# Performance work log

Hardware: AMD Instinct MI355X
Metric: run time of the kernel (lower is better)

The kernel has to match this reference:

```python
import jax, jax.numpy as jnp
import numpy as np

B, T, D = 2, 2048, 1024
NH, DH = 16, 64  # inner = NH*DH = D
SCALE_INIT = 0.02


def setup_inputs() -> dict:
    key = jax.random.key(0)
    kx, kq, kk, kv, ko = jax.random.split(key, 5)
    return {
        "x": jax.random.normal(kx, (B, T, D), dtype=jnp.float32),
        "Wq": jax.random.normal(kq, (D, NH * DH), dtype=jnp.float32) * SCALE_INIT,
        "Wk": jax.random.normal(kk, (D, NH * DH), dtype=jnp.float32) * SCALE_INIT,
        "Wv": jax.random.normal(kv, (D, NH * DH), dtype=jnp.float32) * SCALE_INIT,
        "Wo": jax.random.normal(ko, (NH * DH, D), dtype=jnp.float32) * SCALE_INIT,
    }


def reference(x, Wq, Wk, Wv, Wo):
    # x: (B, T, D)
    b, t, _ = x.shape

    def split_heads(h):
        # (B, T, NH*DH) -> (B, NH, T, DH)
        return h.reshape(b, t, NH, DH).transpose(0, 2, 1, 3)

    q = split_heads(x @ Wq)
    k = split_heads(x @ Wk)
    v = split_heads(x @ Wv)

    scale = jnp.asarray(1.0 / np.sqrt(DH), dtype=x.dtype)
    # The per-chunk loop in the original is mathematically equivalent to
    # full causal attention: each query row attends to keys with k_pos <= q_pos.
    scores = jnp.einsum("bhqd,bhkd->bhqk", q, k) * scale  # (B, NH, T, T)
    causal_mask = jnp.arange(t)[None, :] > jnp.arange(t)[:, None]  # k_pos > q_pos
    scores = jnp.where(causal_mask, -jnp.inf, scores)
    attn = jax.nn.softmax(scores, axis=-1)
    attn = jnp.nan_to_num(attn)  # matches torch.nan_to_num (no fully-masked rows in causal case)
    o = jnp.einsum("bhqk,bhkd->bhqd", attn, v)  # (B, NH, T, DH)
    o = o.transpose(0, 2, 1, 3).reshape(b, t, NH * DH)  # merge heads
    return o @ Wo  # (B, T, D)
```

## Files before the change

### kernel.cpp

```cpp
#include <hip/hip_runtime.h>
#include <hip/hip_bf16.h>
#include <string.h>

#define Bsz 2
#define Tsz 2048
#define Dsz 1024
#define NHsz 16
#define Msz (Bsz*Tsz)

typedef unsigned short bfu;
typedef __attribute__((ext_vector_type(8))) short short8;
typedef __attribute__((ext_vector_type(4))) short short4v;
typedef __attribute__((ext_vector_type(4))) float floatx4;

__device__ __forceinline__ bfu f2bf(float f) {
  unsigned int u = __builtin_bit_cast(unsigned int, f);
  u += 0x7fffu + ((u >> 16) & 1u);
  return (bfu)(u >> 16);
}

__device__ __forceinline__ float fexp2(float x) {
#if __has_builtin(__builtin_amdgcn_exp2f)
  return __builtin_amdgcn_exp2f(x);
#else
  return exp2f(x);
#endif
}

__device__ __forceinline__ short4v pack4bf(float a, float b, float c_, float d) {
  __hip_bfloat162 h01 = __float22bfloat162_rn(make_float2(a, b));
  __hip_bfloat162 h23 = __float22bfloat162_rn(make_float2(c_, d));
  uint2 uu;
  memcpy(&uu.x, &h01, 4);
  memcpy(&uu.y, &h23, 4);
  return __builtin_bit_cast(short4v, uu);
}

__device__ __forceinline__ short8 pack8bf(float4 a, float4 b) {
  __hip_bfloat162 h0 = __float22bfloat162_rn(make_float2(a.x, a.y));
  __hip_bfloat162 h1 = __float22bfloat162_rn(make_float2(a.z, a.w));
  __hip_bfloat162 h2 = __float22bfloat162_rn(make_float2(b.x, b.y));
  __hip_bfloat162 h3 = __float22bfloat162_rn(make_float2(b.z, b.w));
  uint4 u;
  memcpy(&u.x, &h0, 4); memcpy(&u.y, &h1, 4);
  memcpy(&u.z, &h2, 4); memcpy(&u.w, &h3, 4);
  return __builtin_bit_cast(short8, u);
}

__device__ __forceinline__ void async16(const void* g, void* l) {
  void* gnc = (void*)g;
  __builtin_amdgcn_global_load_lds((__attribute__((address_space(1))) void*)gnc,
                                   (__attribute__((address_space(3))) void*)l,
                                   16, 0, 0);
}

__global__ __launch_bounds__(256) void transpose_w(const float* __restrict__ W0, const float* __restrict__ W1,
                                                   const float* __restrict__ W2, const float* __restrict__ W3,
                                                   bfu* __restrict__ wt) {
  __shared__ float tile[32][33];
  const float* W = blockIdx.z == 0 ? W0 : blockIdx.z == 1 ? W1 : blockIdx.z == 2 ? W2 : W3;
  const float s = (blockIdx.z == 0) ? 0.18033688011112042f : 1.0f;
  bfu* WT = wt + (size_t)blockIdx.z * Dsz * Dsz;
  int tx = threadIdx.x, ty = threadIdx.y;
  int kb = blockIdx.y * 32, nb = blockIdx.x * 32;
#pragma unroll
  for (int i = 0; i < 4; ++i)
    tile[ty + i*8][tx] = W[(size_t)(kb + ty + i*8) * Dsz + nb + tx];
  __syncthreads();
#pragma unroll
  for (int i = 0; i < 4; ++i)
    WT[(size_t)(nb + ty + i*8) * Dsz + kb + tx] = f2bf(tile[tx][ty + i*8] * s);
}

template <bool F32OUT, bool AF32, int NT>
__global__ __launch_bounds__(256) void gemm128(const void* __restrict__ Ain, const bfu* __restrict__ Bt0,
                                               void* __restrict__ C0, int K, int N,
                                               size_t strideB, size_t strideC) {
  constexpr int NJ = NT / 32;
  const int tid = threadIdx.x, wave = tid >> 6, lane = tid & 63;
  const int g = lane >> 4, c = lane & 15;
  const int m0 = blockIdx.y * 128, n0 = blockIdx.x * NT;
  const bfu* Bt = Bt0 + strideB * blockIdx.z;
  __shared__ bfu smem[4096 + NT * 32];
  bfu* As = smem;
  bfu* Bs = smem + 4096;
  floatx4 acc[4][NJ] = {};
  const int srow = lane >> 2, scol = (lane & 3) * 8;
  const bfu* gB = Bt + (size_t)(n0 + srow) * K + scol;
  const int wm = (wave >> 1) * 64, wn = (wave & 1) * (NT / 2);

  short8 areg[2];
  if (AF32) {
#pragma unroll
    for (int cc = 0; cc < 2; ++cc) {
      const float* pa = (const float*)Ain +
          (size_t)(m0 + (wave*2 + cc)*16 + srow) * K + scol;
      areg[cc] = pack8bf(((const float4*)pa)[0], ((const float4*)pa)[1]);
    }
  }
  const bfu* gA = AF32 ? nullptr : (const bfu*)Ain + (size_t)(m0 + srow) * K + scol;

  for (int k0 = 0; k0 < K; k0 += 32) {
    __syncthreads();
#pragma unroll
    for (int cc = 0; cc < 2; ++cc) {
      const int chunk = wave * 2 + cc;
      if (AF32) *(short8*)&As[chunk * 512 + lane * 8] = areg[cc];
      else      async16(gA + (size_t)chunk * 16 * K + k0, &As[chunk * 512]);
    }
#pragma unroll
    for (int cc = 0; cc < NT/64; ++cc) {
      const int chunk = wave * (NT/64) + cc;
      async16(gB + (size_t)chunk * 16 * K + k0, &Bs[chunk * 512]);
    }
    __syncthreads();
    if (AF32 && k0 + 32 < K) {
#pragma unroll
      for (int cc = 0; cc < 2; ++cc) {
        const float* pa = (const float*)Ain +
            (size_t)(m0 + (wave*2 + cc)*16 + srow) * K + (k0 + 32) + scol;
        areg[cc] = pack8bf(((const float4*)pa)[0], ((const float4*)pa)[1]);
      }
    }
    short8 afr[4], bfr[NJ];
#pragma unroll
    for (int t = 0; t < 4; ++t) afr[t] = *(const short8*)&As[(wm + t*16 + c) * 32 + g * 8];
#pragma unroll
    for (int t = 0; t < NJ; ++t) bfr[t] = *(const short8*)&Bs[(wn + t*16 + c) * 32 + g * 8];
#pragma unroll
    for (int i = 0; i < 4; ++i)
#pragma unroll
      for (int j = 0; j < NJ; ++j)
        acc[i][j] = __builtin_amdgcn_mfma_f32_16x16x32_bf16(afr[i], bfr[j], acc[i][j], 0, 0, 0);
  }

  const bool vtrans = (!F32OUT) && (NT == 128) && (blockIdx.z == 2);
  if (vtrans) {
    bfu* vtp = (bfu*)C0 + (size_t)2 * strideC;
#pragma unroll
    for (int p = 0; p < 2; ++p) {
      __syncthreads();
      if ((wave & 1) == p) {
#pragma unroll
        for (int i = 0; i < 4; ++i)
#pragma unroll
          for (int j = 0; j < NJ; ++j) {
            const int nl = j*16 + c;
            const int mg = ((wm + i*16) >> 3) + (g >> 1);
            const int phys = nl * 128 + ((mg ^ (nl & 15)) << 3) + ((g & 1) << 2);
            *(short4v*)&smem[phys] = pack4bf(acc[i][j][0], acc[i][j][1],
                                             acc[i][j][2], acc[i][j][3]);
          }
      }
      __syncthreads();
      const int h_ = (n0 + p * 64) >> 6;
      bfu* dst = vtp + ((size_t)((m0 >> 11) * 16 + h_) * 64) * Tsz + (m0 & 2047);
#pragma unroll
      for (int s = 0; s < 4; ++s) {
        const int nl = s * 16 + (tid >> 4);
        const int me = (tid & 15) << 3;
        const int phys = nl * 128 + (((me >> 3) ^ (nl & 15)) << 3);
        *(short8*)&dst[(size_t)nl * Tsz + me] = *(const short8*)&smem[phys];
      }
    }
    return;
  }

#pragma unroll
  for (int i = 0; i < 4; ++i) {
#pragma unroll
    for (int j = 0; j < NJ; ++j) {
      const int m = m0 + wm + i*16 + g*4;
      const int n = n0 + wn + j*16 + c;
#pragma unroll
      for (int r = 0; r < 4; ++r) {
        float v = acc[i][j][r];
        if (F32OUT) ((float*)C0)[(size_t)(m + r) * N + n] = v;
        else        ((bfu*)C0)[strideC * blockIdx.z + (size_t)(m + r) * N + n] = f2bf(v);
      }
    }
  }
}

__global__ __launch_bounds__(256, 2) void attn_kernel(const bfu* __restrict__ qkv,
                                                      bfu* __restrict__ obuf) {
  const int tid = threadIdx.x, wave = tid >> 6, lane = tid & 63;
  const int g = (lane >> 4) & 3, c = lane & 15, c7 = c & 7;

  const int flat = (int)blockIdx.y * 16 + (int)blockIdx.x;
  const int xcd = flat & 7, r_ = flat >> 3;
  const int s = r_ & 3, j0 = r_ >> 2;
  const int bh = xcd * 4 + s;
  const int b = bh >> 4, h = bh & 15;

  const size_t hbq = (size_t)b * Tsz * Dsz + h * 64;
  const bfu* Qp = qkv + hbq;
  const bfu* Kp = qkv + (size_t)Msz * Dsz + hbq;
  const bfu* Vt = qkv + (size_t)2 * Msz * Dsz + (size_t)bh * 64 * Tsz;

  __shared__ bfu Ks[2][64 * 64];
  __shared__ bfu Vs[2][64 * 64];

  const int srow8 = lane >> 3;
  const int soff = ((lane & 7) ^ srow8) << 3;
  const floatx4 z4 = {0.0f, 0.0f, 0.0f, 0.0f};

  for (int hf = 0; hf < 2; ++hf) {
    const int j = hf ? (31 - j0) : j0;
    const int qw = j * 64 + wave * 16;

    short8 bq[2];
#pragma unroll
    for (int kk = 0; kk < 2; ++kk)
      bq[kk] = *(const short8*)(Qp + (size_t)(qw + c) * Dsz + kk * 32 + g * 8);

    const bfu* kpp[2]; const bfu* vpp[2];
#pragma unroll
    for (int cc = 0; cc < 2; ++cc) {
      const int ch = wave * 2 + cc;
      kpp[cc] = Kp + (size_t)(ch * 8 + srow8) * Dsz + soff;
      vpp[cc] = Vt + (size_t)(ch * 8 + srow8) * Tsz + soff;
    }

    floatx4 acc[4] = {};
    float mi = -3.0e38f, li = 0.0f;

#pragma unroll
    for (int cc = 0; cc < 2; ++cc) {
      const int ch = wave * 2 + cc;
      async16(kpp[cc], &Ks[0][ch * 512]);
      async16(vpp[cc], &Vs[0][ch * 512]);
      kpp[cc] += (size_t)64 * Dsz;
      vpp[cc] += 64;
    }

    for (int kt = 0; kt <= j; ++kt) {
      const int cur = kt & 1;
      if (kt < j) {
#pragma unroll
        for (int cc = 0; cc < 2; ++cc) {
          const int ch = wave * 2 + cc;
          async16(kpp[cc], &Ks[cur ^ 1][ch * 512]);
          async16(vpp[cc], &Vs[cur ^ 1][ch * 512]);
          kpp[cc] += (size_t)64 * Dsz;
          vpp[cc] += 64;
        }
        asm volatile("s_waitcnt vmcnt(4)" ::: "memory");
      } else {
        asm volatile("s_waitcnt vmcnt(0)" ::: "memory");
      }
      __builtin_amdgcn_s_barrier();
      asm volatile("" ::: "memory");

      const bfu* KsC = &Ks[cur][0];
      const bfu* VsC = &Vs[cur][0];

      floatx4 st[4];
      __builtin_amdgcn_s_setprio(1);
#pragma unroll
      for (int mk = 0; mk < 4; ++mk) {
        const short8 kf = *(const short8*)&KsC[(mk * 16 + c) * 64 + ((g ^ c7) << 3)];
        st[mk] = __builtin_amdgcn_mfma_f32_16x16x32_bf16(kf, bq[0], z4, 0, 0, 0);
      }
#pragma unroll
      for (int mk = 0; mk < 4; ++mk) {
        const short8 kf = *(const short8*)&KsC[(mk * 16 + c) * 64 + (((4 + g) ^ c7) << 3)];
        st[mk] = __builtin_amdgcn_mfma_f32_16x16x32_bf16(kf, bq[1], st[mk], 0, 0, 0);
      }
      __builtin_amdgcn_s_setprio(0);

      if (kt == j) {
#pragma unroll
        for (int mk = 0; mk < 4; ++mk) {
          const int keyb = kt * 64 + mk * 16 + g * 4;
#pragma unroll
          for (int r = 0; r < 4; ++r)
            if (keyb + r > qw + c) st[mk][r] = -1.0e38f;
        }
      }

      float mloc = -3.0e38f;
#pragma unroll
      for (int mk = 0; mk < 4; ++mk)
        mloc = fmaxf(mloc, fmaxf(fmaxf(st[mk][0], st[mk][1]),
                                 fmaxf(st[mk][2], st[mk][3])));
      const bool resc = !__all(mloc <= mi + 8.0f);
      if (resc) {
        float mr = fmaxf(mloc, __shfl_xor(mloc, 16));
        mr = fmaxf(mr, __shfl_xor(mr, 32));
        const float mnew = fmaxf(mi, mr);
        const float alpha = fexp2(mi - mnew);
        li *= alpha;
        mi = mnew;
        float al[4];
#pragma unroll
        for (int rr = 0; rr < 4; ++rr) al[rr] = __shfl(alpha, (lane & 48) | (g * 4 + rr));
#pragma unroll
        for (int nd = 0; nd < 4; ++nd)
#pragma unroll
          for (int rr = 0; rr < 4; ++rr) acc[nd][rr] *= al[rr];
      }
      short4v pa[4];
#pragma unroll
      for (int mk = 0; mk < 4; ++mk) {
        const float p0 = fexp2(st[mk][0] - mi);
        const float p1 = fexp2(st[mk][1] - mi);
        const float p2 = fexp2(st[mk][2] - mi);
        const float p3 = fexp2(st[mk][3] - mi);
        li += (p0 + p1) + (p2 + p3);
        pa[mk] = pack4bf(p0, p1, p2, p3);
      }

      __builtin_amdgcn_s_setprio(1);
#pragma unroll
      for (int mk = 0; mk < 4; ++mk)
#pragma unroll
        for (int nd = 0; nd < 4; ++nd) {
          const short4v vf = *(const short4v*)&VsC[(nd * 16 + c) * 64 +
              ((((mk << 1) + (g >> 1)) ^ c7) << 3) + ((g & 1) << 2)];
          acc[nd] = __builtin_amdgcn_mfma_f32_16x16x16bf16_1k(pa[mk], vf, acc[nd], 0, 0, 0);
        }
      __builtin_amdgcn_s_setprio(0);

      asm volatile("" ::: "memory");
      __builtin_amdgcn_s_barrier();
      asm volatile("" ::: "memory");
    }

    float lt = li;
    lt += __shfl_xor(lt, 16);
    lt += __shfl_xor(lt, 32);
#pragma unroll
    for (int rr = 0; rr < 4; ++rr) {
      const float inv = 1.0f / __shfl(lt, (lane & 48) | (g * 4 + rr));
#pragma unroll
      for (int nd = 0; nd < 4; ++nd)
        obuf[(size_t)(b * Tsz + qw + g * 4 + rr) * Dsz + h * 64 + nd * 16 + c] =
            f2bf(acc[nd][rr] * inv);
    }
  }
}

extern "C" void kernel_launch(void* const* d_in, const int* in_sizes, int n_in,
                              void* d_out, int out_size, void* d_ws, size_t ws_size,
                              hipStream_t stream) {
  const float* x  = (const float*)d_in[0];
  const float* Wq = (const float*)d_in[1];
  const float* Wk = (const float*)d_in[2];
  const float* Wv = (const float*)d_in[3];
  const float* Wo = (const float*)d_in[4];
  float* out = (float*)d_out;

  bfu* wt   = (bfu*)d_ws;
  bfu* qkv  = wt  + (size_t)4 * Dsz * Dsz;
  bfu* obuf = qkv + (size_t)3 * Msz * Dsz;

  transpose_w<<<dim3(32, 32, 4), dim3(32, 8), 0, stream>>>(Wq, Wk, Wv, Wo, wt);
  gemm128<false, true, 128><<<dim3(Dsz / 128, Msz / 128, 3), dim3(256), 0, stream>>>(
      (const void*)x, wt, (void*)qkv, Dsz, Dsz, (size_t)Dsz * Dsz, (size_t)Msz * Dsz);
  attn_kernel<<<dim3(16, 32), dim3(256), 0, stream>>>(qkv, obuf);
  gemm128<true, false, 64><<<dim3(Dsz / 64, Msz / 128, 1), dim3(256), 0, stream>>>(
      (const void*)obuf, wt + (size_t)3 * Dsz * Dsz, (void*)out, Dsz, Dsz,
      (size_t)0, (size_t)0);
}
```

Baseline: 193.2 us.

## Split attention KV range across two blocks and merge partial softmax results

Doubles the attention grid by giving each query tile two blocks that take alternating key tiles. Each block writes fp32 partial outputs plus its running max and sum, and a new merge kernel combines them into the bf16 buffer. It also adds a separate pass that converts x to bf16 so the QKV GEMM loads A asynchronously, and raises the attention occupancy hint to 4. The aim is more parallelism and occupancy in attention, at the cost of two extra launches and extra fp32 traffic to global memory.

```diff
diff --git a/kernel.cpp b/kernel.cpp
--- a/kernel.cpp
+++ b/kernel.cpp
@@ -54,6 +54,13 @@
                                    16, 0, 0);
 }
 
+__global__ __launch_bounds__(256) void xcvt(const float* __restrict__ x, bfu* __restrict__ xb) {
+  const size_t i = ((size_t)blockIdx.x * 256 + threadIdx.x) * 8;
+  float4 a = *(const float4*)(x + i);
+  float4 b = *(const float4*)(x + i + 4);
+  *(short8*)(xb + i) = pack8bf(a, b);
+}
+
 __global__ __launch_bounds__(256) void transpose_w(const float* __restrict__ W0, const float* __restrict__ W1,
                                                    const float* __restrict__ W2, const float* __restrict__ W3,
                                                    bfu* __restrict__ wt) {
@@ -72,8 +79,8 @@
     WT[(size_t)(nb + ty + i*8) * Dsz + kb + tx] = f2bf(tile[tx][ty + i*8] * s);
 }
 
-template <bool F32OUT, bool AF32, int NT>
-__global__ __launch_bounds__(256) void gemm128(const void* __restrict__ Ain, const bfu* __restrict__ Bt0,
+template <bool F32OUT, int NT>
+__global__ __launch_bounds__(256) void gemm128(const bfu* __restrict__ Ain, const bfu* __restrict__ Bt0,
                                                void* __restrict__ C0, int K, int N,
                                                size_t strideB, size_t strideC) {
   constexpr int NJ = NT / 32;
@@ -88,25 +95,14 @@
   const int srow = lane >> 2, scol = (lane & 3) * 8;
   const bfu* gB = Bt + (size_t)(n0 + srow) * K + scol;
   const int wm = (wave >> 1) * 64, wn = (wave & 1) * (NT / 2);
-
-  short8 areg[2];
-  if (AF32) {
-#pragma unroll
-    for (int cc = 0; cc < 2; ++cc) {
-      const float* pa = (const float*)Ain +
-          (size_t)(m0 + (wave*2 + cc)*16 + srow) * K + scol;
-      areg[cc] = pack8bf(((const float4*)pa)[0], ((const float4*)pa)[1]);
-    }
-  }
-  const bfu* gA = AF32 ? nullptr : (const bfu*)Ain + (size_t)(m0 + srow) * K + scol;
+  const bfu* gA = Ain + (size_t)(m0 + srow) * K + scol;
 
   for (int k0 = 0; k0 < K; k0 += 32) {
     __syncthreads();
 #pragma unroll
     for (int cc = 0; cc < 2; ++cc) {
       const int chunk = wave * 2 + cc;
-      if (AF32) *(short8*)&As[chunk * 512 + lane * 8] = areg[cc];
-      else      async16(gA + (size_t)chunk * 16 * K + k0, &As[chunk * 512]);
+      async16(gA + (size_t)chunk * 16 * K + k0, &As[chunk * 512]);
     }
 #pragma unroll
     for (int cc = 0; cc < NT/64; ++cc) {
@@ -114,14 +110,6 @@
       async16(gB + (size_t)chunk * 16 * K + k0, &Bs[chunk * 512]);
     }
     __syncthreads();
-    if (AF32 && k0 + 32 < K) {
-#pragma unroll
-      for (int cc = 0; cc < 2; ++cc) {
-        const float* pa = (const float*)Ain +
-            (size_t)(m0 + (wave*2 + cc)*16 + srow) * K + (k0 + 32) + scol;
-        areg[cc] = pack8bf(((const float4*)pa)[0], ((const float4*)pa)[1]);
-      }
-    }
     short8 afr[4], bfr[NJ];
 #pragma unroll
     for (int t = 0; t < 4; ++t) afr[t] = *(const short8*)&As[(wm + t*16 + c) * 32 + g * 8];
@@ -182,14 +170,17 @@
   }
 }
 
-__global__ __launch_bounds__(256, 2) void attn_kernel(const bfu* __restrict__ qkv,
-                                                      bfu* __restrict__ obuf) {
+__global__ __launch_bounds__(256, 4) void attn_kernel(const bfu* __restrict__ qkv,
+                                                      float* __restrict__ op0,
+                                                      float* __restrict__ op1,
+                                                      float2* __restrict__ ml) {
   const int tid = threadIdx.x, wave = tid >> 6, lane = tid & 63;
   const int g = (lane >> 4) & 3, c = lane & 15, c7 = c & 7;
 
-  const int flat = (int)blockIdx.y * 16 + (int)blockIdx.x;
+  const int flat = (int)blockIdx.y * 32 + (int)blockIdx.x;
   const int xcd = flat & 7, r_ = flat >> 3;
-  const int s = r_ & 3, j0 = r_ >> 2;
+  const int ksplit = r_ & 1;
+  const int s = (r_ >> 1) & 3, j0 = r_ >> 3;
   const int bh = xcd * 4 + s;
   const int b = bh >> 4, h = bh & 15;
 
@@ -197,6 +188,7 @@
   const bfu* Qp = qkv + hbq;
   const bfu* Kp = qkv + (size_t)Msz * Dsz + hbq;
   const bfu* Vt = qkv + (size_t)2 * Msz * Dsz + (size_t)bh * 64 * Tsz;
+  float* op = ksplit ? op1 : op0;
 
   __shared__ bfu Ks[2][64 * 64];
   __shared__ bfu Vs[2][64 * 64];
@@ -214,117 +206,120 @@
     for (int kk = 0; kk < 2; ++kk)
       bq[kk] = *(const short8*)(Qp + (size_t)(qw + c) * Dsz + kk * 32 + g * 8);
 
-    const bfu* kpp[2]; const bfu* vpp[2];
-#pragma unroll
-    for (int cc = 0; cc < 2; ++cc) {
-      const int ch = wave * 2 + cc;
-      kpp[cc] = Kp + (size_t)(ch * 8 + srow8) * Dsz + soff;
-      vpp[cc] = Vt + (size_t)(ch * 8 + srow8) * Tsz + soff;
-    }
-
     floatx4 acc[4] = {};
     float mi = -3.0e38f, li = 0.0f;
 
-#pragma unroll
-    for (int cc = 0; cc < 2; ++cc) {
-      const int ch = wave * 2 + cc;
-      async16(kpp[cc], &Ks[0][ch * 512]);
-      async16(vpp[cc], &Vs[0][ch * 512]);
-      kpp[cc] += (size_t)64 * Dsz;
-      vpp[cc] += 64;
-    }
-
-    for (int kt = 0; kt <= j; ++kt) {
-      const int cur = kt & 1;
-      if (kt < j) {
-#pragma unroll
-        for (int cc = 0; cc < 2; ++cc) {
-          const int ch = wave * 2 + cc;
-          async16(kpp[cc], &Ks[cur ^ 1][ch * 512]);
-          async16(vpp[cc], &Vs[cur ^ 1][ch * 512]);
-          kpp[cc] += (size_t)64 * Dsz;
-          vpp[cc] += 64;
-        }
-        asm volatile("s_waitcnt vmcnt(4)" ::: "memory");
-      } else {
-        asm volatile("s_waitcnt vmcnt(0)" ::: "memory");
-      }
-      __builtin_amdgcn_s_barrier();
-      asm volatile("" ::: "memory");
-
-      const bfu* KsC = &Ks[cur][0];
-      const bfu* VsC = &Vs[cur][0];
-
-      floatx4 st[4];
-      __builtin_amdgcn_s_setprio(1);
-#pragma unroll
-      for (int mk = 0; mk < 4; ++mk) {
-        const short8 kf = *(const short8*)&KsC[(mk * 16 + c) * 64 + ((g ^ c7) << 3)];
-        st[mk] = __builtin_amdgcn_mfma_f32_16x16x32_bf16(kf, bq[0], z4, 0, 0, 0);
-      }
-#pragma unroll
-      for (int mk = 0; mk < 4; ++mk) {
-        const short8 kf = *(const short8*)&KsC[(mk * 16 + c) * 64 + (((4 + g) ^ c7) << 3)];
-        st[mk] = __builtin_amdgcn_mfma_f32_16x16x32_bf16(kf, bq[1], st[mk], 0, 0, 0);
-      }
-      __builtin_amdgcn_s_setprio(0);
-
-      if (kt == j) {
+    if (ksplit <= j) {
+      const bfu* kpp[2]; const bfu* vpp[2];
+#pragma unroll
+      for (int cc = 0; cc < 2; ++cc) {
+        const int ch = wave * 2 + cc;
+        kpp[cc] = Kp + (size_t)(ksplit * 64 + ch * 8 + srow8) * Dsz + soff;
+        vpp[cc] = Vt + (size_t)(ch * 8 + srow8) * Tsz + ksplit * 64 + soff;
+      }
+
+#pragma unroll
+      for (int cc = 0; cc < 2; ++cc) {
+        const int ch = wave * 2 + cc;
+        async16(kpp[cc], &Ks[0][ch * 512]);
+        async16(vpp[cc], &Vs[0][ch * 512]);
+        kpp[cc] += (size_t)128 * Dsz;
+        vpp[cc] += 128;
+      }
+
+      int cur = 0;
+      for (int kt = ksplit; kt <= j; kt += 2) {
+        if (kt + 2 <= j) {
+#pragma unroll
+          for (int cc = 0; cc < 2; ++cc) {
+            const int ch = wave * 2 + cc;
+            async16(kpp[cc], &Ks[cur ^ 1][ch * 512]);
+            async16(vpp[cc], &Vs[cur ^ 1][ch * 512]);
+            kpp[cc] += (size_t)128 * Dsz;
+            vpp[cc] += 128;
+          }
+          asm volatile("s_waitcnt vmcnt(4)" ::: "memory");
+        } else {
+          asm volatile("s_waitcnt vmcnt(0)" ::: "memory");
+        }
+        __builtin_amdgcn_s_barrier();
+        asm volatile("" ::: "memory");
+
+        const bfu* KsC = &Ks[cur][0];
+        const bfu* VsC = &Vs[cur][0];
+
+        floatx4 st[4];
+        __builtin_amdgcn_s_setprio(1);
 #pragma unroll
         for (int mk = 0; mk < 4; ++mk) {
-          const int keyb = kt * 64 + mk * 16 + g * 4;
-#pragma unroll
-          for (int r = 0; r < 4; ++r)
-            if (keyb + r > qw + c) st[mk][r] = -1.0e38f;
-        }
-      }
-
-      float mloc = -3.0e38f;
-#pragma unroll
-      for (int mk = 0; mk < 4; ++mk)
-        mloc = fmaxf(mloc, fmaxf(fmaxf(st[mk][0], st[mk][1]),
-                                 fmaxf(st[mk][2], st[mk][3])));
-      const bool resc = !__all(mloc <= mi + 8.0f);
-      if (resc) {
-        float mr = fmaxf(mloc, __shfl_xor(mloc, 16));
-        mr = fmaxf(mr, __shfl_xor(mr, 32));
-        const float mnew = fmaxf(mi, mr);
-        const float alpha = fexp2(mi - mnew);
-        li *= alpha;
-        mi = mnew;
-        float al[4];
-#pragma unroll
-        for (int rr = 0; rr < 4; ++rr) al[rr] = __shfl(alpha, (lane & 48) | (g * 4 + rr));
-#pragma unroll
-        for (int nd = 0; nd < 4; ++nd)
-#pragma unroll
-          for (int rr = 0; rr < 4; ++rr) acc[nd][rr] *= al[rr];
-      }
-      short4v pa[4];
-#pragma unroll
-      for (int mk = 0; mk < 4; ++mk) {
-        const float p0 = fexp2(st[mk][0] - mi);
-        const float p1 = fexp2(st[mk][1] - mi);
-        const float p2 = fexp2(st[mk][2] - mi);
-        const float p3 = fexp2(st[mk][3] - mi);
-        li += (p0 + p1) + (p2 + p3);
-        pa[mk] = pack4bf(p0, p1, p2, p3);
-      }
-
-      __builtin_amdgcn_s_setprio(1);
-#pragma unroll
-      for (int mk = 0; mk < 4; ++mk)
-#pragma unroll
-        for (int nd = 0; nd < 4; ++nd) {
-          const short4v vf = *(const short4v*)&VsC[(nd * 16 + c) * 64 +
-              ((((mk << 1) + (g >> 1)) ^ c7) << 3) + ((g & 1) << 2)];
-          acc[nd] = __builtin_amdgcn_mfma_f32_16x16x16bf16_1k(pa[mk], vf, acc[nd], 0, 0, 0);
-        }
-      __builtin_amdgcn_s_setprio(0);
-
-      asm volatile("" ::: "memory");
-      __builtin_amdgcn_s_barrier();
-      asm volatile("" ::: "memory");
+          const short8 kf = *(const short8*)&KsC[(mk * 16 + c) * 64 + ((g ^ c7) << 3)];
+          st[mk] = __builtin_amdgcn_mfma_f32_16x16x32_bf16(kf, bq[0], z4, 0, 0, 0);
+        }
+#pragma unroll
+        for (int mk = 0; mk < 4; ++mk) {
+          const short8 kf = *(const short8*)&KsC[(mk * 16 + c) * 64 + (((4 + g) ^ c7) << 3)];
+          st[mk] = __builtin_amdgcn_mfma_f32_16x16x32_bf16(kf, bq[1], st[mk], 0, 0, 0);
+        }
+        __builtin_amdgcn_s_setprio(0);
+
+        if (kt == j) {
+#pragma unroll
+          for (int mk = 0; mk < 4; ++mk) {
+            const int keyb = kt * 64 + mk * 16 + g * 4;
+#pragma unroll
+            for (int r = 0; r < 4; ++r)
+              if (keyb + r > qw + c) st[mk][r] = -1.0e38f;
+          }
+        }
+
+        float mloc = -3.0e38f;
+#pragma unroll
+        for (int mk = 0; mk < 4; ++mk)
+          mloc = fmaxf(mloc, fmaxf(fmaxf(st[mk][0], st[mk][1]),
+                                   fmaxf(st[mk][2], st[mk][3])));
+        const bool resc = !__all(mloc <= mi + 8.0f);
+        if (resc) {
+          float mr = fmaxf(mloc, __shfl_xor(mloc, 16));
+          mr = fmaxf(mr, __shfl_xor(mr, 32));
+          const float mnew = fmaxf(mi, mr);
+          const float alpha = fexp2(mi - mnew);
+          li *= alpha;
+          mi = mnew;
+          float al[4];
+#pragma unroll
+          for (int rr = 0; rr < 4; ++rr) al[rr] = __shfl(alpha, (lane & 48) | (g * 4 + rr));
+#pragma unroll
+          for (int nd = 0; nd < 4; ++nd)
+#pragma unroll
+            for (int rr = 0; rr < 4; ++rr) acc[nd][rr] *= al[rr];
+        }
+        short4v pa[4];
+#pragma unroll
+        for (int mk = 0; mk < 4; ++mk) {
+          const float p0 = fexp2(st[mk][0] - mi);
+          const float p1 = fexp2(st[mk][1] - mi);
+          const float p2 = fexp2(st[mk][2] - mi);
+          const float p3 = fexp2(st[mk][3] - mi);
+          li += (p0 + p1) + (p2 + p3);
+          pa[mk] = pack4bf(p0, p1, p2, p3);
+        }
+
+        __builtin_amdgcn_s_setprio(1);
+#pragma unroll
+        for (int mk = 0; mk < 4; ++mk)
+#pragma unroll
+          for (int nd = 0; nd < 4; ++nd) {
+            const short4v vf = *(const short4v*)&VsC[(nd * 16 + c) * 64 +
+                ((((mk << 1) + (g >> 1)) ^ c7) << 3) + ((g & 1) << 2)];
+            acc[nd] = __builtin_amdgcn_mfma_f32_16x16x16bf16_1k(pa[mk], vf, acc[nd], 0, 0, 0);
+          }
+        __builtin_amdgcn_s_setprio(0);
+
+        asm volatile("" ::: "memory");
+        __builtin_amdgcn_s_barrier();
+        asm volatile("" ::: "memory");
+        cur ^= 1;
+      }
     }
 
     float lt = li;
@@ -332,13 +327,42 @@
     lt += __shfl_xor(lt, 32);
 #pragma unroll
     for (int rr = 0; rr < 4; ++rr) {
-      const float inv = 1.0f / __shfl(lt, (lane & 48) | (g * 4 + rr));
+      const float lr = __shfl(lt, (lane & 48) | (g * 4 + rr));
+      const float inv = lr > 0.0f ? 1.0f / lr : 0.0f;
 #pragma unroll
       for (int nd = 0; nd < 4; ++nd)
-        obuf[(size_t)(b * Tsz + qw + g * 4 + rr) * Dsz + h * 64 + nd * 16 + c] =
-            f2bf(acc[nd][rr] * inv);
-    }
+        op[(size_t)(b * Tsz + qw + g * 4 + rr) * Dsz + h * 64 + nd * 16 + c] =
+            acc[nd][rr] * inv;
+    }
+    if (lane < 16)
+      ml[(size_t)ksplit * 65536 + bh * 2048 + qw + c] = make_float2(mi, lt);
   }
+}
+
+__global__ __launch_bounds__(256) void merge_split(const float* __restrict__ o0,
+                                                   const float* __restrict__ o1,
+                                                   const float2* __restrict__ ml,
+                                                   bfu* __restrict__ ob) {
+  const int idx = blockIdx.x * 256 + threadIdx.x;
+  const int row = idx >> 7, ch = idx & 127;
+  const int b = row >> 11, q = row & 2047;
+  const int bh = b * 16 + (ch >> 3);
+  const float2 a0 = ml[bh * 2048 + q];
+  const float2 a1 = ml[65536 + bh * 2048 + q];
+  const float M = fmaxf(a0.x, a1.x);
+  const float w0 = fexp2(a0.x - M) * a0.y;
+  const float w1 = fexp2(a1.x - M) * a1.y;
+  const float inv = 1.0f / (w0 + w1);
+  const float u0 = w0 * inv, u1 = w1 * inv;
+  const size_t off = (size_t)row * 1024 + ch * 8;
+  float4 p0 = *(const float4*)(o0 + off), q0 = *(const float4*)(o0 + off + 4);
+  float4 p1 = *(const float4*)(o1 + off), q1 = *(const float4*)(o1 + off + 4);
+  float4 ra, rb;
+  ra.x = u0*p0.x + u1*p1.x; ra.y = u0*p0.y + u1*p1.y;
+  ra.z = u0*p0.z + u1*p1.z; ra.w = u0*p0.w + u1*p1.w;
+  rb.x = u0*q0.x + u1*q1.x; rb.y = u0*q0.y + u1*q1.y;
+  rb.z = u0*q0.z + u1*q1.z; rb.w = u0*q0.w + u1*q1.w;
+  *(short8*)(ob + off) = pack8bf(ra, rb);
 }
 
 extern "C" void kernel_launch(void* const* d_in, const int* in_sizes, int n_in,
@@ -351,15 +375,20 @@
   const float* Wo = (const float*)d_in[4];
   float* out = (float*)d_out;
 
-  bfu* wt   = (bfu*)d_ws;
-  bfu* qkv  = wt  + (size_t)4 * Dsz * Dsz;
-  bfu* obuf = qkv + (size_t)3 * Msz * Dsz;
+  bfu* wt    = (bfu*)d_ws;
+  bfu* qkv   = wt + (size_t)4 * Dsz * Dsz;
+  bfu* obuf  = qkv + (size_t)3 * Msz * Dsz;
+  float* op0 = (float*)(obuf + (size_t)Msz * Dsz);
+  float* op1 = op0 + (size_t)Msz * Dsz;
+  float2* ml = (float2*)(op1 + (size_t)Msz * Dsz);
 
   transpose_w<<<dim3(32, 32, 4), dim3(32, 8), 0, stream>>>(Wq, Wk, Wv, Wo, wt);
-  gemm128<false, true, 128><<<dim3(Dsz / 128, Msz / 128, 3), dim3(256), 0, stream>>>(
-      (const void*)x, wt, (void*)qkv, Dsz, Dsz, (size_t)Dsz * Dsz, (size_t)Msz * Dsz);
-  attn_kernel<<<dim3(16, 32), dim3(256), 0, stream>>>(qkv, obuf);
-  gemm128<true, false, 64><<<dim3(Dsz / 64, Msz / 128, 1), dim3(256), 0, stream>>>(
-      (const void*)obuf, wt + (size_t)3 * Dsz * Dsz, (void*)out, Dsz, Dsz,
+  xcvt<<<dim3(2048), dim3(256), 0, stream>>>(x, obuf);
+  gemm128<false, 128><<<dim3(Dsz / 128, Msz / 128, 3), dim3(256), 0, stream>>>(
+      obuf, wt, (void*)qkv, Dsz, Dsz, (size_t)Dsz * Dsz, (size_t)Msz * Dsz);
+  attn_kernel<<<dim3(32, 32), dim3(256), 0, stream>>>(qkv, op0, op1, ml);
+  merge_split<<<dim3(2048), dim3(256), 0, stream>>>(op0, op1, ml, obuf);
+  gemm128<true, 64><<<dim3(Dsz / 64, Msz / 128, 1), dim3(256), 0, stream>>>(
+      obuf, wt + (size_t)3 * Dsz * Dsz, (void*)out, Dsz, Dsz,
       (size_t)0, (size_t)0);
 }
```

New measurement: 195.9 us. About the same (+1.4%).
